# Optimization experiments

Measured on AMD Instinct MI355X. Metric: run time of the kernel, lower is better.

The kernel has to match this reference:

```python
import jax, jax.numpy as jnp
import numpy as np
from jax import lax

THRESHOLD_ABS = 0.5
MIN_DISTANCE = 3
MAX_PEAKS = 65536  # fixed-size peak buffer (jit-compatible replacement for torch nonzero)


def setup_inputs() -> dict:
    key = jax.random.key(0)
    belive_map = jax.random.uniform(key, (8, 2, 1024, 1024), dtype=jnp.float32)
    return {"belive_map": belive_map}


def reference(belive_map):
    B, C, H, W = belive_map.shape
    k = 2 * MIN_DISTANCE + 1  # 7
    pad = k // 2
    # max_pool2d(kernel=7, stride=1, padding=3) == sliding-window max with -inf padding
    x_max = lax.reduce_window(
        belive_map, -jnp.inf, lax.max,
        window_dimensions=(1, 1, k, k),
        window_strides=(1, 1, 1, 1),
        padding=((0, 0), (0, 0), (pad, pad), (pad, pad)),
    )
    x_mask = x_max == belive_map
    # exclude_border: zero a band of width 2*min_distance on all four sides
    ex = 2 * MIN_DISTANCE
    x_mask = x_mask.at[..., :ex].set(False)
    x_mask = x_mask.at[..., -ex:].set(False)
    x_mask = x_mask.at[..., :ex, :].set(False)
    x_mask = x_mask.at[..., -ex:, :].set(False)
    x_mask = x_mask & (belive_map > THRESHOLD_ABS)

    mask_flat = x_mask.reshape(B, C * H * W)
    val_flat = belive_map.reshape(B, C * H * W)

    def pick(m, v):
        # fixed-size nonzero; padded entries get index -1
        idx = jnp.nonzero(m, size=MAX_PEAKS, fill_value=-1)[0]
        valid = idx >= 0
        safe = jnp.where(valid, idx, 0)
        scores = jnp.where(valid, v[safe], 0.0)
        c = safe // (H * W)
        rem = safe % (H * W)
        h = rem // W
        w = rem % W
        coords = jnp.stack([w, h], axis=-1)           # (x, y) == ind[:, [2, 1]]
        coords = jnp.where(valid[:, None], coords, -1)
        labels = jnp.where(valid, c + 1, 0)            # ind[:, 0] + 1
        return coords, labels, scores

    coordinates, labels, scores = jax.vmap(pick)(mask_flat, val_flat)
    # per-image (coordinates, labels, scores), batched with fixed MAX_PEAKS slots;
    # invalid slots: coords=-1, labels=0, scores=0
    return coordinates, labels, scores
```

## Files before the change

### kernel.cpp

```cpp
#include <hip/hip_runtime.h>

#define HW  (1024u*1024u)
#define CHW (2u*HW)
#define MAXP 65536u
#define LABEL_OFF 1048576u
#define SCORE_OFF 1572864u
#define NINF (-3.0e38f)
#define PAIRS_PER_CHUNK 512u

__device__ __forceinline__ float max3f(float a, float b, float c) {
    return fmaxf(fmaxf(a, b), c);
}

__global__ __launch_bounds__(256, 4) void mask_kernel(const float* __restrict__ map,
                                                      uint2* __restrict__ pairs,
                                                      unsigned* __restrict__ chunkCount) {
    __shared__ float4 rowbuf[2][2][258];
    __shared__ unsigned swscan[4];
    int bid0 = blockIdx.x;
    int bid = (bid0 & 7) * 128 + (bid0 >> 3);
    int tid = threadIdx.x;
    int stripe = bid & 63;
    int img = bid >> 6;
    int r0 = stripe << 4;
    int lane = tid & 63, wv = tid >> 6;
    const float4* __restrict__ base = (const float4*)(map + ((size_t)img << 20));
    const size_t pbase = (size_t)bid * PAIRS_PER_CHUNK;

    if (tid < 8) {
        float4 n4 = make_float4(NINF, NINF, NINF, NINF);
        rowbuf[(tid >> 2) & 1][(tid >> 1) & 1][(tid & 1) * 257] = n4;
    }

    int c0 = tid * 4;
    int cvm = 0;
    #pragma unroll
    for (int j = 0; j < 4; ++j) {
        int cc = c0 + j;
        if (cc >= 6 && cc <= 1017) cvm |= (1 << j);
    }

    float4 w[12];
    #pragma unroll
    for (int k = 0; k < 10; ++k) {
        int rr = r0 - 3 + k;
        w[k] = ((unsigned)rr < 1024u) ? base[rr * 256 + tid]
                                      : make_float4(NINF, NINF, NINF, NINF);
    }

    unsigned chunkOff = 0;

    #pragma unroll
    for (int p = 0; p < 8; ++p) {
        int rA = r0 + 2 * p;
        if (p < 6) {
            int q1 = rA + 7, q2 = rA + 8;
            w[(2 * p + 10) % 12] = ((unsigned)q1 < 1024u) ? base[q1 * 256 + tid]
                                                          : make_float4(NINF, NINF, NINF, NINF);
            w[(2 * p + 11) % 12] = ((unsigned)q2 < 1024u) ? base[q2 * 256 + tid]
                                                          : make_float4(NINF, NINF, NINF, NINF);
        }
        float4 s0 = w[(2 * p + 0) % 12], s1 = w[(2 * p + 1) % 12];
        float4 s2 = w[(2 * p + 2) % 12], s3 = w[(2 * p + 3) % 12];
        float4 s4 = w[(2 * p + 4) % 12], s5 = w[(2 * p + 5) % 12];
        float4 s6 = w[(2 * p + 6) % 12], s7 = w[(2 * p + 7) % 12];

        float4 c6, vmA, vmB;
        c6.x = fmaxf(max3f(s1.x, s2.x, s3.x), max3f(s4.x, s5.x, s6.x));
        c6.y = fmaxf(max3f(s1.y, s2.y, s3.y), max3f(s4.y, s5.y, s6.y));
        c6.z = fmaxf(max3f(s1.z, s2.z, s3.z), max3f(s4.z, s5.z, s6.z));
        c6.w = fmaxf(max3f(s1.w, s2.w, s3.w), max3f(s4.w, s5.w, s6.w));
        vmA.x = fmaxf(c6.x, s0.x); vmB.x = fmaxf(c6.x, s7.x);
        vmA.y = fmaxf(c6.y, s0.y); vmB.y = fmaxf(c6.y, s7.y);
        vmA.z = fmaxf(c6.z, s0.z); vmB.z = fmaxf(c6.z, s7.z);
        vmA.w = fmaxf(c6.w, s0.w); vmB.w = fmaxf(c6.w, s7.w);

        rowbuf[p & 1][0][tid + 1] = vmA;
        rowbuf[p & 1][1][tid + 1] = vmB;
        __syncthreads();
        float4 LA = rowbuf[p & 1][0][tid], RA = rowbuf[p & 1][0][tid + 2];
        float4 LB = rowbuf[p & 1][1][tid], RB = rowbuf[p & 1][1][tid + 2];

        float mA0 = max3f(max3f(LA.y, LA.z, LA.w),  max3f(vmA.x, vmA.y, vmA.z), vmA.w);
        float mA1 = max3f(max3f(LA.z, LA.w, vmA.x), max3f(vmA.y, vmA.z, vmA.w), RA.x);
        float mA2 = max3f(max3f(LA.w, vmA.x, vmA.y), max3f(vmA.z, vmA.w, RA.x), RA.y);
        float mA3 = max3f(max3f(vmA.x, vmA.y, vmA.z), max3f(vmA.w, RA.x, RA.y), RA.z);
        float mB0 = max3f(max3f(LB.y, LB.z, LB.w),  max3f(vmB.x, vmB.y, vmB.z), vmB.w);
        float mB1 = max3f(max3f(LB.z, LB.w, vmB.x), max3f(vmB.y, vmB.z, vmB.w), RB.x);
        float mB2 = max3f(max3f(LB.w, vmB.x, vmB.y), max3f(vmB.z, vmB.w, RB.x), RB.y);
        float mB3 = max3f(max3f(vmB.x, vmB.y, vmB.z), max3f(vmB.w, RB.x, RB.y), RB.z);

        float4 ctrA = s3, ctrB = s4;
        int fA0 = (ctrA.x == mA0) & (ctrA.x > 0.5f);
        int fA1 = (ctrA.y == mA1) & (ctrA.y > 0.5f);
        int fA2 = (ctrA.z == mA2) & (ctrA.z > 0.5f);
        int fA3 = (ctrA.w == mA3) & (ctrA.w > 0.5f);
        int fB0 = (ctrB.x == mB0) & (ctrB.x > 0.5f);
        int fB1 = (ctrB.y == mB1) & (ctrB.y > 0.5f);
        int fB2 = (ctrB.z == mB2) & (ctrB.z > 0.5f);
        int fB3 = (ctrB.w == mB3) & (ctrB.w > 0.5f);
        int nibA = (fA0 | (fA1 << 1) | (fA2 << 2) | (fA3 << 3)) & cvm;
        int nibB = (fB0 | (fB1 << 1) | (fB2 << 2) | (fB3 << 3)) & cvm;
        int rowokA = (rA >= 6) & (rA <= 1017);
        int rowokB = ((rA + 1) >= 6) & ((rA + 1) <= 1017);
        nibA = rowokA ? nibA : 0;
        nibB = rowokB ? nibB : 0;

        unsigned packed = (unsigned)__popc((unsigned)nibA)
                        | ((unsigned)__popc((unsigned)nibB) << 16);
        unsigned incl = packed;
        #pragma unroll
        for (int off = 1; off < 64; off <<= 1) {
            unsigned nn = __shfl_up(incl, off, 64);
            if (lane >= off) incl += nn;
        }
        if (lane == 63) swscan[wv] = incl;
        __syncthreads();
        unsigned excl = incl - packed;
        unsigned preA = 0, preB = 0, sumA = 0, sumB = 0;
        #pragma unroll
        for (int k = 0; k < 4; ++k) {
            unsigned sv = swscan[k];
            if (k < wv) { preA += sv & 0xFFFFu; preB += sv >> 16; }
            sumA += sv & 0xFFFFu; sumB += sv >> 16;
        }
        unsigned posA = chunkOff + preA + (excl & 0xFFFFu);
        unsigned posB = chunkOff + sumA + preB + (excl >> 16);
        chunkOff += sumA + sumB;

        unsigned flatbase = ((unsigned)(img & 1) << 20) | ((unsigned)rA << 10)
                          | ((unsigned)tid * 4u);
        if (nibA & 1) pairs[pbase + posA++] = make_uint2(flatbase + 0u, __float_as_uint(ctrA.x));
        if (nibA & 2) pairs[pbase + posA++] = make_uint2(flatbase + 1u, __float_as_uint(ctrA.y));
        if (nibA & 4) pairs[pbase + posA++] = make_uint2(flatbase + 2u, __float_as_uint(ctrA.z));
        if (nibA & 8) pairs[pbase + posA++] = make_uint2(flatbase + 3u, __float_as_uint(ctrA.w));
        if (nibB & 1) pairs[pbase + posB++] = make_uint2(flatbase + 1024u, __float_as_uint(ctrB.x));
        if (nibB & 2) pairs[pbase + posB++] = make_uint2(flatbase + 1025u, __float_as_uint(ctrB.y));
        if (nibB & 4) pairs[pbase + posB++] = make_uint2(flatbase + 1026u, __float_as_uint(ctrB.z));
        if (nibB & 8) pairs[pbase + posB++] = make_uint2(flatbase + 1027u, __float_as_uint(ctrB.w));
    }

    if (tid == 0) chunkCount[bid] = chunkOff;
}

__global__ __launch_bounds__(512) void scan_scatter(const uint2* __restrict__ pairs,
                                                    const unsigned* __restrict__ chunkCount,
                                                    float* __restrict__ out) {
    int bid0 = blockIdx.x;
    int blk = (bid0 & 7) * 128 + (bid0 >> 3);
    int b = blk >> 7, cib = blk & 127;
    int tid = threadIdx.x;
    int lane = tid & 63, wv = tid >> 6;

    __shared__ unsigned long long sw[8];
    __shared__ unsigned sbase, stotal;

    unsigned cc = (tid < 128) ? chunkCount[b * 128 + tid] : 0u;
    unsigned long long v = ((tid < cib) ? (unsigned long long)cc : 0ull)
                         | ((unsigned long long)cc << 32);
    for (int off = 32; off; off >>= 1) v += __shfl_down(v, off, 64);
    if (lane == 0) sw[wv] = v;
    __syncthreads();
    if (tid == 0) {
        unsigned long long t = sw[0] + sw[1] + sw[2] + sw[3] + sw[4] + sw[5] + sw[6] + sw[7];
        sbase  = (unsigned)t;
        stotal = (unsigned)(t >> 32);
    }
    __syncthreads();

    unsigned n = chunkCount[blk];
    if (n > PAIRS_PER_CHUNK) n = PAIRS_PER_CHUNK;
    if ((unsigned)tid < n) {
        uint2 pr = pairs[(size_t)blk * PAIRS_PER_CHUNK + tid];
        unsigned slot = sbase + (unsigned)tid;
        if (slot < MAXP) {
            unsigned flat = pr.x;
            unsigned c = flat >> 20;
            unsigned h = (flat >> 10) & 1023u;
            unsigned wcol = flat & 1023u;
            unsigned o = b * MAXP + slot;
            out[2u * o]         = (float)wcol;
            out[2u * o + 1]     = (float)h;
            out[LABEL_OFF + o]  = (float)(c + 1u);
            out[SCORE_OFF + o]  = __uint_as_float(pr.y);
        }
    }

    unsigned slot = ((unsigned)cib) * 512u + (unsigned)tid;
    if (slot >= stotal) {
        unsigned o = b * MAXP + slot;
        float2 neg1; neg1.x = -1.0f; neg1.y = -1.0f;
        ((float2*)out)[o]   = neg1;
        out[LABEL_OFF + o]  = 0.0f;
        out[SCORE_OFF + o]  = 0.0f;
    }
}

extern "C" void kernel_launch(void* const* d_in, const int* in_sizes, int n_in,
                              void* d_out, int out_size, void* d_ws, size_t ws_size,
                              hipStream_t stream) {
    const float* map = (const float*)d_in[0];
    float* out = (float*)d_out;
    uint2* pairs = (uint2*)d_ws;
    unsigned* chunkCount = (unsigned*)((char*)d_ws + 4194304);

    mask_kernel<<<1024, 256, 0, stream>>>(map, pairs, chunkCount);
    scan_scatter<<<1024, 512, 0, stream>>>(pairs, chunkCount, out);
}
```

Baseline: 29.19 us.

## Remove per-row block barrier by deferring cross-wave ordering to scatter kernel

The mask kernel no longer runs a __syncthreads and shared-memory cross-wave scan for every row pair. Each wave now compacts its peaks into its own 128-slot segment and writes per-wave, per-row counts to global memory. The scatter kernel rebuilds row-major order with two small wave-level scans over those counts and remaps each pair to its final slot. This takes eight block barriers out of the mask loop, at the cost of extra count traffic, more index arithmetic in the scatter kernel, and a 128-pair cap per wave segment.

```diff
diff --git a/kernel.cpp b/kernel.cpp
--- a/kernel.cpp
+++ b/kernel.cpp
@@ -6,7 +6,6 @@
 #define LABEL_OFF 1048576u
 #define SCORE_OFF 1572864u
 #define NINF (-3.0e38f)
-#define PAIRS_PER_CHUNK 512u
 
 __device__ __forceinline__ float max3f(float a, float b, float c) {
     return fmaxf(fmaxf(a, b), c);
@@ -14,9 +13,10 @@
 
 __global__ __launch_bounds__(256, 4) void mask_kernel(const float* __restrict__ map,
                                                       uint2* __restrict__ pairs,
+                                                      unsigned* __restrict__ counts,
                                                       unsigned* __restrict__ chunkCount) {
     __shared__ float4 rowbuf[2][2][258];
-    __shared__ unsigned swscan[4];
+    __shared__ unsigned sred[4];
     int bid0 = blockIdx.x;
     int bid = (bid0 & 7) * 128 + (bid0 >> 3);
     int tid = threadIdx.x;
@@ -25,7 +25,7 @@
     int r0 = stripe << 4;
     int lane = tid & 63, wv = tid >> 6;
     const float4* __restrict__ base = (const float4*)(map + ((size_t)img << 20));
-    const size_t pbase = (size_t)bid * PAIRS_PER_CHUNK;
+    const size_t pbase = (size_t)bid * 512u + (size_t)wv * 128u;
 
     if (tid < 8) {
         float4 n4 = make_float4(NINF, NINF, NINF, NINF);
@@ -48,7 +48,7 @@
                                       : make_float4(NINF, NINF, NINF, NINF);
     }
 
-    unsigned chunkOff = 0;
+    unsigned woff = 0;
 
     #pragma unroll
     for (int p = 0; p < 8; ++p) {
@@ -114,36 +114,33 @@
             unsigned nn = __shfl_up(incl, off, 64);
             if (lane >= off) incl += nn;
         }
-        if (lane == 63) swscan[wv] = incl;
-        __syncthreads();
+        if (lane == 63) counts[bid * 32 + wv * 8 + p] = incl;
+        unsigned tot = __shfl(incl, 63, 64);
         unsigned excl = incl - packed;
-        unsigned preA = 0, preB = 0, sumA = 0, sumB = 0;
-        #pragma unroll
-        for (int k = 0; k < 4; ++k) {
-            unsigned sv = swscan[k];
-            if (k < wv) { preA += sv & 0xFFFFu; preB += sv >> 16; }
-            sumA += sv & 0xFFFFu; sumB += sv >> 16;
-        }
-        unsigned posA = chunkOff + preA + (excl & 0xFFFFu);
-        unsigned posB = chunkOff + sumA + preB + (excl >> 16);
-        chunkOff += sumA + sumB;
+        unsigned sumA = tot & 0xFFFFu;
+        unsigned posA = woff + (excl & 0xFFFFu);
+        unsigned posB = woff + sumA + (excl >> 16);
+        woff += sumA + (tot >> 16);
 
         unsigned flatbase = ((unsigned)(img & 1) << 20) | ((unsigned)rA << 10)
                           | ((unsigned)tid * 4u);
-        if (nibA & 1) pairs[pbase + posA++] = make_uint2(flatbase + 0u, __float_as_uint(ctrA.x));
-        if (nibA & 2) pairs[pbase + posA++] = make_uint2(flatbase + 1u, __float_as_uint(ctrA.y));
-        if (nibA & 4) pairs[pbase + posA++] = make_uint2(flatbase + 2u, __float_as_uint(ctrA.z));
-        if (nibA & 8) pairs[pbase + posA++] = make_uint2(flatbase + 3u, __float_as_uint(ctrA.w));
-        if (nibB & 1) pairs[pbase + posB++] = make_uint2(flatbase + 1024u, __float_as_uint(ctrB.x));
-        if (nibB & 2) pairs[pbase + posB++] = make_uint2(flatbase + 1025u, __float_as_uint(ctrB.y));
-        if (nibB & 4) pairs[pbase + posB++] = make_uint2(flatbase + 1026u, __float_as_uint(ctrB.z));
-        if (nibB & 8) pairs[pbase + posB++] = make_uint2(flatbase + 1027u, __float_as_uint(ctrB.w));
-    }
-
-    if (tid == 0) chunkCount[bid] = chunkOff;
+        if (nibA & 1) { if (posA < 128u) pairs[pbase + posA] = make_uint2(flatbase + 0u, __float_as_uint(ctrA.x)); posA++; }
+        if (nibA & 2) { if (posA < 128u) pairs[pbase + posA] = make_uint2(flatbase + 1u, __float_as_uint(ctrA.y)); posA++; }
+        if (nibA & 4) { if (posA < 128u) pairs[pbase + posA] = make_uint2(flatbase + 2u, __float_as_uint(ctrA.z)); posA++; }
+        if (nibA & 8) { if (posA < 128u) pairs[pbase + posA] = make_uint2(flatbase + 3u, __float_as_uint(ctrA.w)); posA++; }
+        if (nibB & 1) { if (posB < 128u) pairs[pbase + posB] = make_uint2(flatbase + 1024u, __float_as_uint(ctrB.x)); posB++; }
+        if (nibB & 2) { if (posB < 128u) pairs[pbase + posB] = make_uint2(flatbase + 1025u, __float_as_uint(ctrB.y)); posB++; }
+        if (nibB & 4) { if (posB < 128u) pairs[pbase + posB] = make_uint2(flatbase + 1026u, __float_as_uint(ctrB.z)); posB++; }
+        if (nibB & 8) { if (posB < 128u) pairs[pbase + posB] = make_uint2(flatbase + 1027u, __float_as_uint(ctrB.w)); posB++; }
+    }
+
+    if (lane == 0) sred[wv] = woff;
+    __syncthreads();
+    if (tid == 0) chunkCount[bid] = sred[0] + sred[1] + sred[2] + sred[3];
 }
 
 __global__ __launch_bounds__(512) void scan_scatter(const uint2* __restrict__ pairs,
+                                                    const unsigned* __restrict__ counts,
                                                     const unsigned* __restrict__ chunkCount,
                                                     float* __restrict__ out) {
     int bid0 = blockIdx.x;
@@ -154,6 +151,16 @@
 
     __shared__ unsigned long long sw[8];
     __shared__ unsigned sbase, stotal;
+    __shared__ unsigned short cnt16[16][4];
+    __shared__ unsigned short dstS[64];
+    __shared__ unsigned short segS[64];
+
+    if (tid < 32) {
+        unsigned cv = counts[blk * 32 + tid];
+        int seg = tid >> 3, p = tid & 7;
+        cnt16[2 * p][seg]     = (unsigned short)(cv & 0xFFFFu);
+        cnt16[2 * p + 1][seg] = (unsigned short)(cv >> 16);
+    }
 
     unsigned cc = (tid < 128) ? chunkCount[b * 128 + tid] : 0u;
     unsigned long long v = ((tid < cib) ? (unsigned long long)cc : 0ull)
@@ -166,15 +173,38 @@
         sbase  = (unsigned)t;
         stotal = (unsigned)(t >> 32);
     }
+
+    if (wv == 0) {
+        unsigned val = cnt16[lane >> 2][lane & 3];
+        unsigned incl = val;
+        #pragma unroll
+        for (int off = 1; off < 64; off <<= 1) {
+            unsigned nn = __shfl_up(incl, off, 64);
+            if (lane >= off) incl += nn;
+        }
+        dstS[lane] = (unsigned short)(incl - val);
+    } else if (wv == 1) {
+        unsigned val = cnt16[lane & 15][lane >> 4];
+        unsigned incl = val;
+        #pragma unroll
+        for (int off = 1; off < 64; off <<= 1) {
+            unsigned nn = __shfl_up(incl, off, 64);
+            if (lane >= off) incl += nn;
+        }
+        segS[lane] = (unsigned short)(incl - val);
+    }
     __syncthreads();
 
-    unsigned n = chunkCount[blk];
-    if (n > PAIRS_PER_CHUNK) n = PAIRS_PER_CHUNK;
-    if ((unsigned)tid < n) {
-        uint2 pr = pairs[(size_t)blk * PAIRS_PER_CHUNK + tid];
-        unsigned slot = sbase + (unsigned)tid;
+    int seg = tid >> 7, idx = tid & 127;
+    unsigned segBase = segS[seg * 16];
+    unsigned segTot  = (unsigned)segS[seg * 16 + 15] + (unsigned)cnt16[15][seg] - segBase;
+    if ((unsigned)idx < segTot) {
+        uint2 pr = pairs[(size_t)blk * 512u + (size_t)seg * 128u + idx];
+        unsigned flat = pr.x;
+        unsigned row = (flat >> 10) & 15u;
+        unsigned slot = sbase + (unsigned)dstS[row * 4 + seg]
+                      + (unsigned)idx - ((unsigned)segS[seg * 16 + row] - segBase);
         if (slot < MAXP) {
-            unsigned flat = pr.x;
             unsigned c = flat >> 20;
             unsigned h = (flat >> 10) & 1023u;
             unsigned wcol = flat & 1023u;
@@ -202,8 +232,9 @@
     const float* map = (const float*)d_in[0];
     float* out = (float*)d_out;
     uint2* pairs = (uint2*)d_ws;
-    unsigned* chunkCount = (unsigned*)((char*)d_ws + 4194304);
-
-    mask_kernel<<<1024, 256, 0, stream>>>(map, pairs, chunkCount);
-    scan_scatter<<<1024, 512, 0, stream>>>(pairs, chunkCount, out);
-}
+    unsigned* counts = (unsigned*)((char*)d_ws + 4194304);
+    unsigned* chunkCount = (unsigned*)((char*)d_ws + 4325376);
+
+    mask_kernel<<<1024, 256, 0, stream>>>(map, pairs, counts, chunkCount);
+    scan_scatter<<<1024, 512, 0, stream>>>(pairs, counts, chunkCount, out);
+}
```

Measured after the change: 30.38 us. 4.1% more time.

## Compute per-batch chunk prefix scan in last-finishing mask block

Applied to the files above, without the earlier changes.

The per-chunk prefix sum over chunk counts moves out of every scan_scatter block and into the last mask_kernel block of each batch, chosen with a done counter incremented by an atomic. scan_scatter then only reads a precomputed base and total, which drops two block barriers and the redundant 128-element reduction from each of its 1024 blocks. In exchange it adds an atomic per mask block, a serialized tail scan in one block per batch, and an extra memset launch to reset the counters.

```diff
diff --git a/kernel.cpp b/kernel.cpp
--- a/kernel.cpp
+++ b/kernel.cpp
@@ -14,9 +14,13 @@
 
 __global__ __launch_bounds__(256, 4) void mask_kernel(const float* __restrict__ map,
                                                       uint2* __restrict__ pairs,
-                                                      unsigned* __restrict__ chunkCount) {
+                                                      unsigned* chunkCount,
+                                                      unsigned* __restrict__ chunkBase,
+                                                      unsigned* __restrict__ batchTotal,
+                                                      unsigned* doneCtr) {
     __shared__ float4 rowbuf[2][2][258];
     __shared__ unsigned swscan[4];
+    __shared__ int sIsLast;
     int bid0 = blockIdx.x;
     int bid = (bid0 & 7) * 128 + (bid0 >> 3);
     int tid = threadIdx.x;
@@ -140,39 +144,58 @@
         if (nibB & 8) pairs[pbase + posB++] = make_uint2(flatbase + 1027u, __float_as_uint(ctrB.w));
     }
 
-    if (tid == 0) chunkCount[bid] = chunkOff;
+    int b = bid >> 7;
+    if (tid == 0) {
+        chunkCount[bid] = chunkOff;
+        unsigned old = __hip_atomic_fetch_add(&doneCtr[b], 1u,
+                                              __ATOMIC_ACQ_REL, __HIP_MEMORY_SCOPE_AGENT);
+        sIsLast = (old == 127u);
+    }
+    __syncthreads();
+
+    if (sIsLast && tid < 64) {
+        unsigned cA = __hip_atomic_load(&chunkCount[b * 128 + lane],
+                                        __ATOMIC_RELAXED, __HIP_MEMORY_SCOPE_AGENT);
+        unsigned cB = __hip_atomic_load(&chunkCount[b * 128 + 64 + lane],
+                                        __ATOMIC_RELAXED, __HIP_MEMORY_SCOPE_AGENT);
+        unsigned iA = cA;
+        #pragma unroll
+        for (int off = 1; off < 64; off <<= 1) {
+            unsigned nn = __shfl_up(iA, off, 64);
+            if (lane >= off) iA += nn;
+        }
+        unsigned tA = __shfl(iA, 63, 64);
+        unsigned iB = cB;
+        #pragma unroll
+        for (int off = 1; off < 64; off <<= 1) {
+            unsigned nn = __shfl_up(iB, off, 64);
+            if (lane >= off) iB += nn;
+        }
+        unsigned tB = __shfl(iB, 63, 64);
+        chunkBase[b * 128 + lane]      = iA - cA;
+        chunkBase[b * 128 + 64 + lane] = tA + iB - cB;
+        if (lane == 0) batchTotal[b] = tA + tB;
+    }
 }
 
 __global__ __launch_bounds__(512) void scan_scatter(const uint2* __restrict__ pairs,
                                                     const unsigned* __restrict__ chunkCount,
+                                                    const unsigned* __restrict__ chunkBase,
+                                                    const unsigned* __restrict__ batchTotal,
                                                     float* __restrict__ out) {
     int bid0 = blockIdx.x;
     int blk = (bid0 & 7) * 128 + (bid0 >> 3);
     int b = blk >> 7, cib = blk & 127;
     int tid = threadIdx.x;
-    int lane = tid & 63, wv = tid >> 6;
-
-    __shared__ unsigned long long sw[8];
-    __shared__ unsigned sbase, stotal;
-
-    unsigned cc = (tid < 128) ? chunkCount[b * 128 + tid] : 0u;
-    unsigned long long v = ((tid < cib) ? (unsigned long long)cc : 0ull)
-                         | ((unsigned long long)cc << 32);
-    for (int off = 32; off; off >>= 1) v += __shfl_down(v, off, 64);
-    if (lane == 0) sw[wv] = v;
-    __syncthreads();
-    if (tid == 0) {
-        unsigned long long t = sw[0] + sw[1] + sw[2] + sw[3] + sw[4] + sw[5] + sw[6] + sw[7];
-        sbase  = (unsigned)t;
-        stotal = (unsigned)(t >> 32);
-    }
-    __syncthreads();
-
-    unsigned n = chunkCount[blk];
+
+    unsigned base  = chunkBase[blk];
+    unsigned n     = chunkCount[blk];
+    unsigned total = batchTotal[b];
     if (n > PAIRS_PER_CHUNK) n = PAIRS_PER_CHUNK;
+
     if ((unsigned)tid < n) {
         uint2 pr = pairs[(size_t)blk * PAIRS_PER_CHUNK + tid];
-        unsigned slot = sbase + (unsigned)tid;
+        unsigned slot = base + (unsigned)tid;
         if (slot < MAXP) {
             unsigned flat = pr.x;
             unsigned c = flat >> 20;
@@ -187,7 +210,7 @@
     }
 
     unsigned slot = ((unsigned)cib) * 512u + (unsigned)tid;
-    if (slot >= stotal) {
+    if (slot >= total) {
         unsigned o = b * MAXP + slot;
         float2 neg1; neg1.x = -1.0f; neg1.y = -1.0f;
         ((float2*)out)[o]   = neg1;
@@ -201,9 +224,15 @@
                               hipStream_t stream) {
     const float* map = (const float*)d_in[0];
     float* out = (float*)d_out;
-    uint2* pairs = (uint2*)d_ws;
+    uint2*    pairs      = (uint2*)d_ws;
     unsigned* chunkCount = (unsigned*)((char*)d_ws + 4194304);
-
-    mask_kernel<<<1024, 256, 0, stream>>>(map, pairs, chunkCount);
-    scan_scatter<<<1024, 512, 0, stream>>>(pairs, chunkCount, out);
-}
+    unsigned* chunkBase  = (unsigned*)((char*)d_ws + 4198400);
+    unsigned* batchTotal = (unsigned*)((char*)d_ws + 4202496);
+    unsigned* doneCtr    = (unsigned*)((char*)d_ws + 4202528);
+
+    hipMemsetAsync(doneCtr, 0, 32, stream);
+    mask_kernel<<<1024, 256, 0, stream>>>(map, pairs, chunkCount,
+                                          chunkBase, batchTotal, doneCtr);
+    scan_scatter<<<1024, 512, 0, stream>>>(pairs, chunkCount, chunkBase,
+                                           batchTotal, out);
+}
```

Measured after the change: 62.24 us. 113% more time.
